# Performance work log

Hardware: AMD Instinct MI355X
Metric: run time of the kernel (lower is better)

## Reference

```python
import jax, jax.numpy as jnp
import numpy as np

VOCAB = 10000
HID = 256

def setup_inputs() -> dict:
    key = jax.random.key(0)
    ks = jax.random.split(key, 7)
    B, T = 64, 64
    input_data = jax.random.randint(ks[0], (B, T), 0, VOCAB, dtype=jnp.int32)
    targets = jax.random.randint(ks[1], (B, T), 0, VOCAB, dtype=jnp.int32)
    # Xavier-ish scaled params
    E = jax.random.normal(ks[2], (VOCAB, HID), dtype=jnp.float32) * (1.0 / np.sqrt(HID))
    W_lstm = jax.random.normal(ks[3], (2 * HID, 4 * HID), dtype=jnp.float32) * (1.0 / np.sqrt(2 * HID))
    b_lstm = jnp.zeros((4 * HID,), dtype=jnp.float32)
    W_dense = jax.random.normal(ks[4], (HID, VOCAB), dtype=jnp.float32) * (1.0 / np.sqrt(HID))
    b_dense = jnp.zeros((VOCAB,), dtype=jnp.float32)
    return {"input_data": input_data, "targets": targets, "E": E,
            "W_lstm": W_lstm, "b_lstm": b_lstm, "W_dense": W_dense, "b_dense": b_dense}

def lstm_scan(xs, W, b, h0, c0):
    # xs: [T, B, H] time-major. TF LSTMCell: gates = [x,h]@W + b, order i,j,f,o, forget_bias=1.0
    def step(carry, x):
        h, c = carry
        gates = jnp.concatenate([x, h], axis=-1) @ W + b  # [B, 4H]
        i, j, f, o = jnp.split(gates, 4, axis=-1)
        c_new = jax.nn.sigmoid(f + 1.0) * c + jax.nn.sigmoid(i) * jnp.tanh(j)
        h_new = jax.nn.sigmoid(o) * jnp.tanh(c_new)
        return (h_new, c_new), h_new
    (hT, cT), hs = jax.lax.scan(step, (h0, c0), xs)
    return hs, (hT, cT)

def reference(input_data, targets, E, W_lstm, b_lstm, W_dense, b_dense):
    B, T = input_data.shape
    inputs = E[input_data]                       # [B, T, H] embedding lookup (no dropout: eval)
    xs = jnp.transpose(inputs, (1, 0, 2))        # [T, B, H]
    h0 = jnp.zeros((B, HID), dtype=E.dtype)
    c0 = jnp.zeros((B, HID), dtype=E.dtype)
    hs, _ = lstm_scan(xs, W_lstm, b_lstm, h0, c0)  # [T, B, H]
    outputs = jnp.transpose(hs, (1, 0, 2))       # [B, T, H]
    logits = outputs @ W_dense + b_dense         # [B, T, V]
    logp = jax.nn.log_softmax(logits, axis=-1)
    ce = -jnp.take_along_axis(logp, targets[..., None].astype(jnp.int32), axis=-1)[..., 0]  # [B, T]
    perplexity = jnp.exp(ce)                     # elementwise, as in add_loss_op
    return perplexity
```

## Files before the change

### kernel.cpp

```cpp
#include <hip/hip_runtime.h>
#include <math.h>

#define VOCABN 10000
#define HIDN   256
#define GATES  1024
#define BN     64
#define TN     64
#define BT     4096
#define NCT    625

typedef unsigned int       u32;
typedef unsigned short     u16;
typedef unsigned long long u64;
typedef float v4f __attribute__((ext_vector_type(4)));
typedef short v8s __attribute__((ext_vector_type(8)));

__device__ __forceinline__ float bf2f(u16 u) {
    return __uint_as_float(((u32)u) << 16);
}
__device__ __forceinline__ u16 f2bf(float f) {
    u32 u = __float_as_uint(f);
    u += 0x7FFFu + ((u >> 16) & 1u);
    return (u16)(u >> 16);
}
__device__ __forceinline__ float fast_sigmoid(float x) {
    return 1.0f / (1.0f + __expf(-x));
}
__device__ __forceinline__ float fast_tanh(float x) {
    float e = __expf(-2.0f * fabsf(x));
    float t = (1.0f - e) / (1.0f + e);
    return copysignf(t, x);
}

__global__ __launch_bounds__(256) void k_wfrag(
    const float* __restrict__ src,
    u16*         __restrict__ dst,
    int ncols)
{
    __shared__ u16 lt[HIDN][16];
    const int c = blockIdx.x;
    const int t = threadIdx.x;
    const float* s = src + (size_t)t * ncols + c * 16;
    #pragma unroll
    for (int j4 = 0; j4 < 4; ++j4) {
        float4 v = *(const float4*)(s + j4 * 4);
        lt[t][j4*4+0] = f2bf(v.x);
        lt[t][j4*4+1] = f2bf(v.y);
        lt[t][j4*4+2] = f2bf(v.z);
        lt[t][j4*4+3] = f2bf(v.w);
    }
    __syncthreads();
    #pragma unroll
    for (int h = 0; h < 2; ++h) {
        int f = t + h * 256;
        int q = f >> 6, l = f & 63;
        int m = l & 15, kb = q * 32 + ((l >> 4) & 3) * 8;
        u32 w[4];
        #pragma unroll
        for (int j = 0; j < 4; ++j)
            w[j] = (u32)lt[kb + 2*j][m] | ((u32)lt[kb + 2*j + 1][m] << 16);
        *(uint4*)(dst + (((size_t)c * 8 + q) * 64 + l) * 8) =
            make_uint4(w[0], w[1], w[2], w[3]);
    }
}

__global__ __launch_bounds__(256) void k_xgates(
    const int*   __restrict__ idx,
    const float* __restrict__ E,
    const u16*   __restrict__ Wxf,
    const float* __restrict__ bl,
    float*       __restrict__ gx)
{
    const int r0   = blockIdx.x * 16;
    const int tid  = threadIdx.x;
    const int w    = tid >> 6, lane = tid & 63;
    const int m    = lane & 15, quad = lane >> 4;

    v8s a[8];
    {
        const float* e = E + (size_t)idx[r0 + m] * HIDN + quad * 8;
        #pragma unroll
        for (int q = 0; q < 8; ++q) {
            float4 x0 = *(const float4*)(e + q * 32);
            float4 x1 = *(const float4*)(e + q * 32 + 4);
            uint4 t4 = make_uint4(
                (u32)f2bf(x0.x) | ((u32)f2bf(x0.y) << 16),
                (u32)f2bf(x0.z) | ((u32)f2bf(x0.w) << 16),
                (u32)f2bf(x1.x) | ((u32)f2bf(x1.y) << 16),
                (u32)f2bf(x1.z) | ((u32)f2bf(x1.w) << 16));
            a[q] = *(v8s*)&t4;
        }
    }

    for (int c = w; c < GATES / 16; c += 4) {
        v4f acc = {0.f, 0.f, 0.f, 0.f};
        #pragma unroll
        for (int q = 0; q < 8; ++q) {
            v8s b = *(const v8s*)(Wxf + (((size_t)c * 8 + q) * 64 + lane) * 8);
            acc = __builtin_amdgcn_mfma_f32_16x16x32_bf16(a[q], b, acc, 0, 0, 0);
        }
        const int col = c * 16 + m;
        const float bv = bl[col];
        #pragma unroll
        for (int r = 0; r < 4; ++r)
            gx[(size_t)(r0 + quad * 4 + r) * GATES + col] = acc[r] + bv;
    }
}

__global__ __launch_bounds__(256) void k_plstm(
    const u16*   __restrict__ Whf,
    const float* __restrict__ gx,
    u16*                      Hx,
    u16*         __restrict__ Hb,
    u32*                      bar)
{
    __shared__ uint4 Wl4[4 * 512];
    __shared__ float gl[4][16][16];

    const int tid  = threadIdx.x;
    const int rg   = blockIdx.x >> 4;
    const int ns   = blockIdx.x & 15;
    const int u0   = ns * 16;
    const int w    = tid >> 6;
    const int lane = tid & 63;
    const int m    = lane & 15, kq = lane >> 4;

    {
        const uint4* src = (const uint4*)Whf;
        #pragma unroll
        for (int i = 0; i < 8; ++i) {
            int e  = tid + i * 256;
            int ct = e >> 9, off = e & 511;
            Wl4[e] = src[(size_t)(ct * 16 + ns) * 512 + off];
        }
    }
    {
        float* g0 = (float*)gl;
        #pragma unroll
        for (int j = 0; j < 4; ++j) g0[tid * 4 + j] = 0.0f;
    }
    __syncthreads();

    const u16* Wl = (const u16*)Wl4;

    const int r = tid >> 4, u = tid & 15;
    const int b = rg * 16 + r;
    const float* gxp = gx + (size_t)b * TN * GATES + u0 + u;
    u16* hbp = Hb + (size_t)b * TN * HIDN + u0 + u;
    const int hxw = b * HIDN + u0 + u;
    const int aoff = (rg * 16 + m) * HIDN + kq * 8;

    float cst = 0.0f;
    float4 gxr;
    gxr.x = gxp[0]; gxr.y = gxp[256]; gxr.z = gxp[512]; gxr.w = gxp[768];

    for (int t = 0; t < TN; ++t) {
        float4 gxn = gxr;
        if (t + 1 < TN) {
            const float* p = gxp + (size_t)(t + 1) * GATES;
            gxn.x = p[0]; gxn.y = p[256]; gxn.z = p[512]; gxn.w = p[768];
        }

        if (t > 0) {
            const u64* hsrc = (const u64*)(Hx + (t & 1) * (BN * HIDN) + aoff);
            v4f acc = {0.f, 0.f, 0.f, 0.f};
            #pragma unroll
            for (int q = 0; q < 8; ++q) {
                union { u64 d[2]; v8s v; } av;
                av.d[0] = __hip_atomic_load(hsrc + q * 8,     __ATOMIC_RELAXED,
                                            __HIP_MEMORY_SCOPE_AGENT);
                av.d[1] = __hip_atomic_load(hsrc + q * 8 + 1, __ATOMIC_RELAXED,
                                            __HIP_MEMORY_SCOPE_AGENT);
                v8s bf = *(const v8s*)(Wl + ((w * 8 + q) * 64 + lane) * 8);
                acc = __builtin_amdgcn_mfma_f32_16x16x32_bf16(av.v, bf, acc, 0, 0, 0);
            }
            #pragma unroll
            for (int rr = 0; rr < 4; ++rr)
                gl[w][kq * 4 + rr][m] = acc[rr];
        }
        __syncthreads();

        {
            float ai = gl[0][r][u] + gxr.x;
            float aj = gl[1][r][u] + gxr.y;
            float af = gl[2][r][u] + gxr.z;
            float ao = gl[3][r][u] + gxr.w;
            float ig = fast_sigmoid(ai);
            float fg = fast_sigmoid(af + 1.0f);
            float og = fast_sigmoid(ao);
            float jt = fast_tanh(aj);
            cst = fg * cst + ig * jt;
            float hn = og * fast_tanh(cst);
            u32 hv = f2bf(hn);
            hbp[(size_t)t * HIDN] = (u16)hv;

            if (t + 1 < TN) {
                u32 p1 = __shfl_down(hv, 1);
                u32 p2 = __shfl_down(hv, 2);
                u32 p3 = __shfl_down(hv, 3);
                if ((tid & 3) == 0) {
                    u64 pk = (u64)(hv | (p1 << 16))
                           | ((u64)(p2 | (p3 << 16)) << 32);
                    u64* dst = (u64*)(Hx + (((t & 1) ^ 1) * (BN * HIDN)) + hxw);
                    __hip_atomic_store(dst, pk, __ATOMIC_RELAXED,
                                       __HIP_MEMORY_SCOPE_AGENT);
                }
            }
        }

        if (t + 1 < TN) {
            __syncthreads();
            if (tid == 0) {
                __hip_atomic_fetch_add(&bar[rg * 64], 1u, __ATOMIC_RELAXED,
                                       __HIP_MEMORY_SCOPE_AGENT);
                u32 tgt = (u32)(t + 1) * 16u;
                while (__hip_atomic_load(&bar[rg * 64], __ATOMIC_RELAXED,
                                         __HIP_MEMORY_SCOPE_AGENT) < tgt)
                    __builtin_amdgcn_s_sleep(1);
            }
            __syncthreads();
        }
        gxr = gxn;
    }
}

__global__ __launch_bounds__(256) void k_dense(
    const u16*   __restrict__ Hb,
    const u16*   __restrict__ Wf,
    const float* __restrict__ bd,
    float*       __restrict__ S)
{
    __shared__ float Sl[32];
    const int rg  = blockIdx.x >> 1, hv = blockIdx.x & 1;
    const int r0  = rg * 32;
    const int tid = threadIdx.x;
    const int w   = tid >> 6, lane = tid & 63;
    const int m   = lane & 15, quad = lane >> 4;

    if (tid < 32) Sl[tid] = 0.0f;

    v8s a[2][8];
    #pragma unroll
    for (int rt = 0; rt < 2; ++rt) {
        const u16* hrow = Hb + (size_t)(r0 + rt * 16 + m) * HIDN + quad * 8;
        #pragma unroll
        for (int q = 0; q < 8; ++q)
            a[rt][q] = *(const v8s*)(hrow + q * 32);
    }
    __syncthreads();

    float s[2][4] = {{0.f,0.f,0.f,0.f},{0.f,0.f,0.f,0.f}};
    const int cbeg = hv ? 313 : 0;
    const int cend = hv ? NCT : 313;
    for (int c = cbeg + w; c < cend; c += 4) {
        v4f acc0 = {0.f,0.f,0.f,0.f};
        v4f acc1 = {0.f,0.f,0.f,0.f};
        #pragma unroll
        for (int q = 0; q < 8; ++q) {
            v8s bq = *(const v8s*)(Wf + (((size_t)c * 8 + q) * 64 + lane) * 8);
            acc0 = __builtin_amdgcn_mfma_f32_16x16x32_bf16(a[0][q], bq, acc0, 0, 0, 0);
            acc1 = __builtin_amdgcn_mfma_f32_16x16x32_bf16(a[1][q], bq, acc1, 0, 0, 0);
        }
        float bv = bd[c * 16 + m];
        #pragma unroll
        for (int r = 0; r < 4; ++r) {
            s[0][r] += __expf(acc0[r] + bv);
            s[1][r] += __expf(acc1[r] + bv);
        }
    }

    #pragma unroll
    for (int rt = 0; rt < 2; ++rt)
        #pragma unroll
        for (int r = 0; r < 4; ++r)
            atomicAdd(&Sl[rt * 16 + quad * 4 + r], s[rt][r]);
    __syncthreads();
    if (tid < 32) S[(size_t)hv * BT + r0 + tid] = Sl[tid];
}

__global__ __launch_bounds__(256) void k_target(
    const u16*   __restrict__ Hb,
    const u16*   __restrict__ Wf,
    const float* __restrict__ bd,
    const int*   __restrict__ tgt,
    float*       __restrict__ tl)
{
    const int tid = threadIdx.x;
    const int row = blockIdx.x * 8 + (tid >> 5);
    const int t   = tid & 31;
    const int q   = t >> 2, lq = t & 3;
    const int v   = tgt[row];
    const int c   = v >> 4, vm = v & 15;
    const int kb  = q * 32 + lq * 8;

    v8s h  = *(const v8s*)(Hb + (size_t)row * HIDN + kb);
    v8s wv = *(const v8s*)(Wf + (((size_t)c * 8 + q) * 64 + lq * 16 + vm) * 8);
    float acc = 0.0f;
    #pragma unroll
    for (int j = 0; j < 8; ++j)
        acc = fmaf(bf2f((u16)h[j]), bf2f((u16)wv[j]), acc);
    #pragma unroll
    for (int off = 16; off >= 1; off >>= 1)
        acc += __shfl_down(acc, off, 32);
    if (t == 0) tl[row] = acc + bd[v];
}

__global__ __launch_bounds__(256) void k_final(
    const float* __restrict__ S,
    const float* __restrict__ tl,
    float*       __restrict__ out)
{
    int i = blockIdx.x * 256 + threadIdx.x;
    out[i] = __expf(__logf(S[i] + S[BT + i]) - tl[i]);
}

extern "C" void kernel_launch(void* const* d_in, const int* in_sizes, int n_in,
                              void* d_out, int out_size, void* d_ws, size_t ws_size,
                              hipStream_t stream) {
    const int*   input   = (const int*)  d_in[0];
    const int*   targets = (const int*)  d_in[1];
    const float* E       = (const float*)d_in[2];
    const float* W_lstm  = (const float*)d_in[3];
    const float* b_lstm  = (const float*)d_in[4];
    const float* W_dense = (const float*)d_in[5];
    const float* b_dense = (const float*)d_in[6];
    float* out = (float*)d_out;

    char* ws = (char*)d_ws;
    float* gx  = (float*)ws;
    u16*   Wf  = (u16*)ws;
    u16*   Hb  = (u16*)(ws + ((size_t)16 << 20));
    u16*   Whf = (u16*)(ws + ((size_t)18 << 20));
    u16*   Wxf = (u16*)(ws + ((size_t)18 << 20) + ((size_t)512 << 10));
    u16*   Hx  = (u16*)(ws + ((size_t)19 << 20));
    float* S   = (float*)(ws + ((size_t)19 << 20) + ((size_t)64 << 10));
    float* tl  = (float*)(ws + ((size_t)19 << 20) + ((size_t)96 << 10));
    u32*   bar = (u32*)  (ws + ((size_t)19 << 20) + ((size_t)112 << 10));

    hipMemsetAsync(bar, 0, 1024, stream);
    k_wfrag <<<64,      256, 0, stream>>>(W_lstm,                      Wxf, GATES);
    k_wfrag <<<64,      256, 0, stream>>>(W_lstm + (size_t)HIDN*GATES, Whf, GATES);
    k_xgates<<<BT / 16, 256, 0, stream>>>(input, E, Wxf, b_lstm, gx);
    k_plstm <<<64,      256, 0, stream>>>(Whf, gx, Hx, Hb, bar);
    k_wfrag <<<NCT,     256, 0, stream>>>(W_dense, Wf, VOCABN);
    k_dense <<<256,     256, 0, stream>>>(Hb, Wf, b_dense, S);
    k_target<<<BT / 8,  256, 0, stream>>>(Hb, Wf, b_dense, targets, tl);
    k_final <<<BT / 256,256, 0, stream>>>(S, tl, out);
}
```

Measured before the change: 423.4 us.

## Merge weight prep kernels, store x-gates in bf16, fuse target logit into dense

The three weight-fragment conversions now run in one kernel launch. The precomputed input gates are stored as bf16 instead of fp32, halving their traffic into the recurrent kernel. The target-logit kernel is removed: the dense kernel records the target logit as it computes each column. It also drops the sleep in the barrier spin and remaps dense block indices. The aim is fewer launches and less memory traffic, at the cost of lower gate precision and busier barrier polling.

```diff
diff --git a/kernel.cpp b/kernel.cpp
--- a/kernel.cpp
+++ b/kernel.cpp
@@ -31,15 +31,17 @@
     float t = (1.0f - e) / (1.0f + e);
     return copysignf(t, x);
 }
-
-__global__ __launch_bounds__(256) void k_wfrag(
-    const float* __restrict__ src,
-    u16*         __restrict__ dst,
-    int ncols)
-{
-    __shared__ u16 lt[HIDN][16];
-    const int c = blockIdx.x;
-    const int t = threadIdx.x;
+__device__ __forceinline__ u64 llc_load(const u64* p) {
+    return __hip_atomic_load(p, __ATOMIC_RELAXED, __HIP_MEMORY_SCOPE_AGENT);
+}
+__device__ __forceinline__ void llc_store(u64* p, u64 v) {
+    __hip_atomic_store(p, v, __ATOMIC_RELAXED, __HIP_MEMORY_SCOPE_AGENT);
+}
+
+__device__ __forceinline__ void wfrag_dev(
+    const float* __restrict__ src, u16* __restrict__ dst, int ncols, int c,
+    int t, u16 lt[HIDN][16])
+{
     const float* s = src + (size_t)t * ncols + c * 16;
     #pragma unroll
     for (int j4 = 0; j4 < 4; ++j4) {
@@ -64,12 +66,28 @@
     }
 }
 
-__global__ __launch_bounds__(256) void k_xgates(
+__global__ __launch_bounds__(256) void k_prep1(
+    const float* __restrict__ W_lstm,
+    const float* __restrict__ W_dense,
+    u16* __restrict__ Wxf, u16* __restrict__ Whf, u16* __restrict__ Wf)
+{
+    __shared__ u16 lt[HIDN][16];
+    const int bid = blockIdx.x;
+    if (bid < 64)
+        wfrag_dev(W_lstm, Wxf, GATES, bid, threadIdx.x, lt);
+    else if (bid < 128)
+        wfrag_dev(W_lstm + (size_t)HIDN * GATES, Whf, GATES, bid - 64,
+                  threadIdx.x, lt);
+    else
+        wfrag_dev(W_dense, Wf, VOCABN, bid - 128, threadIdx.x, lt);
+}
+
+__global__ __launch_bounds__(256) void k_prep2(
     const int*   __restrict__ idx,
     const float* __restrict__ E,
     const u16*   __restrict__ Wxf,
     const float* __restrict__ bl,
-    float*       __restrict__ gx)
+    u16*         __restrict__ gxb)
 {
     const int r0   = blockIdx.x * 16;
     const int tid  = threadIdx.x;
@@ -91,7 +109,6 @@
             a[q] = *(v8s*)&t4;
         }
     }
-
     for (int c = w; c < GATES / 16; c += 4) {
         v4f acc = {0.f, 0.f, 0.f, 0.f};
         #pragma unroll
@@ -103,13 +120,13 @@
         const float bv = bl[col];
         #pragma unroll
         for (int r = 0; r < 4; ++r)
-            gx[(size_t)(r0 + quad * 4 + r) * GATES + col] = acc[r] + bv;
+            gxb[(size_t)(r0 + quad * 4 + r) * GATES + col] = f2bf(acc[r] + bv);
     }
 }
 
 __global__ __launch_bounds__(256) void k_plstm(
     const u16*   __restrict__ Whf,
-    const float* __restrict__ gx,
+    const u16*   __restrict__ gxb,
     u16*                      Hx,
     u16*         __restrict__ Hb,
     u32*                      bar)
@@ -145,20 +162,24 @@
 
     const int r = tid >> 4, u = tid & 15;
     const int b = rg * 16 + r;
-    const float* gxp = gx + (size_t)b * TN * GATES + u0 + u;
+    const u16* gxp = gxb + (size_t)b * TN * GATES + u0 + u;
     u16* hbp = Hb + (size_t)b * TN * HIDN + u0 + u;
     const int hxw = b * HIDN + u0 + u;
     const int aoff = (rg * 16 + m) * HIDN + kq * 8;
 
-    float cst = 0.0f;
-    float4 gxr;
-    gxr.x = gxp[0]; gxr.y = gxp[256]; gxr.z = gxp[512]; gxr.w = gxp[768];
+    float cstate = 0.0f;
+    float gr[4], gn[4];
+    #pragma unroll
+    for (int g = 0; g < 4; ++g) gr[g] = bf2f(gxp[g * 256]);
 
     for (int t = 0; t < TN; ++t) {
-        float4 gxn = gxr;
         if (t + 1 < TN) {
-            const float* p = gxp + (size_t)(t + 1) * GATES;
-            gxn.x = p[0]; gxn.y = p[256]; gxn.z = p[512]; gxn.w = p[768];
+            const u16* p = gxp + (size_t)(t + 1) * GATES;
+            #pragma unroll
+            for (int g = 0; g < 4; ++g) gn[g] = bf2f(p[g * 256]);
+        } else {
+            #pragma unroll
+            for (int g = 0; g < 4; ++g) gn[g] = gr[g];
         }
 
         if (t > 0) {
@@ -167,10 +188,8 @@
             #pragma unroll
             for (int q = 0; q < 8; ++q) {
                 union { u64 d[2]; v8s v; } av;
-                av.d[0] = __hip_atomic_load(hsrc + q * 8,     __ATOMIC_RELAXED,
-                                            __HIP_MEMORY_SCOPE_AGENT);
-                av.d[1] = __hip_atomic_load(hsrc + q * 8 + 1, __ATOMIC_RELAXED,
-                                            __HIP_MEMORY_SCOPE_AGENT);
+                av.d[0] = llc_load(hsrc + q * 8);
+                av.d[1] = llc_load(hsrc + q * 8 + 1);
                 v8s bf = *(const v8s*)(Wl + ((w * 8 + q) * 64 + lane) * 8);
                 acc = __builtin_amdgcn_mfma_f32_16x16x32_bf16(av.v, bf, acc, 0, 0, 0);
             }
@@ -181,16 +200,16 @@
         __syncthreads();
 
         {
-            float ai = gl[0][r][u] + gxr.x;
-            float aj = gl[1][r][u] + gxr.y;
-            float af = gl[2][r][u] + gxr.z;
-            float ao = gl[3][r][u] + gxr.w;
+            float ai = gl[0][r][u] + gr[0];
+            float aj = gl[1][r][u] + gr[1];
+            float af = gl[2][r][u] + gr[2];
+            float ao = gl[3][r][u] + gr[3];
             float ig = fast_sigmoid(ai);
             float fg = fast_sigmoid(af + 1.0f);
             float og = fast_sigmoid(ao);
             float jt = fast_tanh(aj);
-            cst = fg * cst + ig * jt;
-            float hn = og * fast_tanh(cst);
+            cstate = fg * cstate + ig * jt;
+            float hn = og * fast_tanh(cstate);
             u32 hv = f2bf(hn);
             hbp[(size_t)t * HIDN] = (u16)hv;
 
@@ -202,8 +221,7 @@
                     u64 pk = (u64)(hv | (p1 << 16))
                            | ((u64)(p2 | (p3 << 16)) << 32);
                     u64* dst = (u64*)(Hx + (((t & 1) ^ 1) * (BN * HIDN)) + hxw);
-                    __hip_atomic_store(dst, pk, __ATOMIC_RELAXED,
-                                       __HIP_MEMORY_SCOPE_AGENT);
+                    llc_store(dst, pk);
                 }
             }
         }
@@ -215,12 +233,12 @@
                                        __HIP_MEMORY_SCOPE_AGENT);
                 u32 tgt = (u32)(t + 1) * 16u;
                 while (__hip_atomic_load(&bar[rg * 64], __ATOMIC_RELAXED,
-                                         __HIP_MEMORY_SCOPE_AGENT) < tgt)
-                    __builtin_amdgcn_s_sleep(1);
+                                         __HIP_MEMORY_SCOPE_AGENT) < tgt) { }
             }
             __syncthreads();
         }
-        gxr = gxn;
+        #pragma unroll
+        for (int g = 0; g < 4; ++g) gr[g] = gn[g];
     }
 }
 
@@ -228,21 +246,26 @@
     const u16*   __restrict__ Hb,
     const u16*   __restrict__ Wf,
     const float* __restrict__ bd,
-    float*       __restrict__ S)
+    const int*   __restrict__ tgt,
+    float*       __restrict__ S,
+    float*       __restrict__ tl)
 {
     __shared__ float Sl[32];
-    const int rg  = blockIdx.x >> 1, hv = blockIdx.x & 1;
+    __shared__ int   tg[32];
+    const int bid = blockIdx.x;
+    const int hv  = (bid >> 2) & 1;
+    const int rg  = (bid >> 3) * 4 + (bid & 3);
     const int r0  = rg * 32;
     const int tid = threadIdx.x;
     const int w   = tid >> 6, lane = tid & 63;
-    const int m   = lane & 15, quad = lane >> 4;
-
-    if (tid < 32) Sl[tid] = 0.0f;
+    const int m   = lane & 15, kq = lane >> 4;
+
+    if (tid < 32) { Sl[tid] = 0.0f; tg[tid] = tgt[r0 + tid]; }
 
     v8s a[2][8];
     #pragma unroll
     for (int rt = 0; rt < 2; ++rt) {
-        const u16* hrow = Hb + (size_t)(r0 + rt * 16 + m) * HIDN + quad * 8;
+        const u16* hrow = Hb + (size_t)(r0 + rt * 16 + m) * HIDN + kq * 8;
         #pragma unroll
         for (int q = 0; q < 8; ++q)
             a[rt][q] = *(const v8s*)(hrow + q * 32);
@@ -261,11 +284,18 @@
             acc0 = __builtin_amdgcn_mfma_f32_16x16x32_bf16(a[0][q], bq, acc0, 0, 0, 0);
             acc1 = __builtin_amdgcn_mfma_f32_16x16x32_bf16(a[1][q], bq, acc1, 0, 0, 0);
         }
-        float bv = bd[c * 16 + m];
-        #pragma unroll
-        for (int r = 0; r < 4; ++r) {
-            s[0][r] += __expf(acc0[r] + bv);
-            s[1][r] += __expf(acc1[r] + bv);
+        const int col = c * 16 + m;
+        const float bv = bd[col];
+        #pragma unroll
+        for (int rt = 0; rt < 2; ++rt) {
+            v4f* ac = rt ? &acc1 : &acc0;
+            #pragma unroll
+            for (int r = 0; r < 4; ++r) {
+                float l = (*ac)[r] + bv;
+                int row = rt * 16 + kq * 4 + r;
+                if (col == tg[row]) tl[r0 + row] = l;
+                s[rt][r] += __expf(l);
+            }
         }
     }
 
@@ -273,36 +303,9 @@
     for (int rt = 0; rt < 2; ++rt)
         #pragma unroll
         for (int r = 0; r < 4; ++r)
-            atomicAdd(&Sl[rt * 16 + quad * 4 + r], s[rt][r]);
+            atomicAdd(&Sl[rt * 16 + kq * 4 + r], s[rt][r]);
     __syncthreads();
     if (tid < 32) S[(size_t)hv * BT + r0 + tid] = Sl[tid];
-}
-
-__global__ __launch_bounds__(256) void k_target(
-    const u16*   __restrict__ Hb,
-    const u16*   __restrict__ Wf,
-    const float* __restrict__ bd,
-    const int*   __restrict__ tgt,
-    float*       __restrict__ tl)
-{
-    const int tid = threadIdx.x;
-    const int row = blockIdx.x * 8 + (tid >> 5);
-    const int t   = tid & 31;
-    const int q   = t >> 2, lq = t & 3;
-    const int v   = tgt[row];
-    const int c   = v >> 4, vm = v & 15;
-    const int kb  = q * 32 + lq * 8;
-
-    v8s h  = *(const v8s*)(Hb + (size_t)row * HIDN + kb);
-    v8s wv = *(const v8s*)(Wf + (((size_t)c * 8 + q) * 64 + lq * 16 + vm) * 8);
-    float acc = 0.0f;
-    #pragma unroll
-    for (int j = 0; j < 8; ++j)
-        acc = fmaf(bf2f((u16)h[j]), bf2f((u16)wv[j]), acc);
-    #pragma unroll
-    for (int off = 16; off >= 1; off >>= 1)
-        acc += __shfl_down(acc, off, 32);
-    if (t == 0) tl[row] = acc + bd[v];
 }
 
 __global__ __launch_bounds__(256) void k_final(
@@ -327,23 +330,20 @@
     float* out = (float*)d_out;
 
     char* ws = (char*)d_ws;
-    float* gx  = (float*)ws;
-    u16*   Wf  = (u16*)ws;
-    u16*   Hb  = (u16*)(ws + ((size_t)16 << 20));
-    u16*   Whf = (u16*)(ws + ((size_t)18 << 20));
-    u16*   Wxf = (u16*)(ws + ((size_t)18 << 20) + ((size_t)512 << 10));
-    u16*   Hx  = (u16*)(ws + ((size_t)19 << 20));
-    float* S   = (float*)(ws + ((size_t)19 << 20) + ((size_t)64 << 10));
-    float* tl  = (float*)(ws + ((size_t)19 << 20) + ((size_t)96 << 10));
-    u32*   bar = (u32*)  (ws + ((size_t)19 << 20) + ((size_t)112 << 10));
+    u16*   gxb = (u16*)ws;
+    u16*   Wf  = (u16*)(ws + ((size_t)8 << 20));
+    u16*   Hb  = (u16*)(ws + ((size_t)13 << 20) + ((size_t)256 << 10));
+    u16*   Whf = (u16*)(ws + ((size_t)15 << 20) + ((size_t)256 << 10));
+    u16*   Wxf = (u16*)(ws + ((size_t)15 << 20) + ((size_t)768 << 10));
+    u16*   Hx  = (u16*)(ws + ((size_t)16 << 20) + ((size_t)256 << 10));
+    float* S   = (float*)(ws + ((size_t)16 << 20) + ((size_t)320 << 10));
+    float* tl  = (float*)(ws + ((size_t)16 << 20) + ((size_t)352 << 10));
+    u32*   bar = (u32*)  (ws + ((size_t)16 << 20) + ((size_t)368 << 10));
 
     hipMemsetAsync(bar, 0, 1024, stream);
-    k_wfrag <<<64,      256, 0, stream>>>(W_lstm,                      Wxf, GATES);
-    k_wfrag <<<64,      256, 0, stream>>>(W_lstm + (size_t)HIDN*GATES, Whf, GATES);
-    k_xgates<<<BT / 16, 256, 0, stream>>>(input, E, Wxf, b_lstm, gx);
-    k_plstm <<<64,      256, 0, stream>>>(Whf, gx, Hx, Hb, bar);
-    k_wfrag <<<NCT,     256, 0, stream>>>(W_dense, Wf, VOCABN);
-    k_dense <<<256,     256, 0, stream>>>(Hb, Wf, b_dense, S);
-    k_target<<<BT / 8,  256, 0, stream>>>(Hb, Wf, b_dense, targets, tl);
-    k_final <<<BT / 256,256, 0, stream>>>(S, tl, out);
-}
+    k_prep1<<<753,      256, 0, stream>>>(W_lstm, W_dense, Wxf, Whf, Wf);
+    k_prep2<<<BT / 16,  256, 0, stream>>>(input, E, Wxf, b_lstm, gxb);
+    k_plstm<<<64,       256, 0, stream>>>(Whf, gxb, Hx, Hb, bar);
+    k_dense<<<256,      256, 0, stream>>>(Hb, Wf, b_dense, targets, S, tl);
+    k_final<<<BT / 256, 256, 0, stream>>>(S, tl, out);
+}
```

Measured after the change: 528.5 us. 1.25x slower.
